# Performance work log

Measured on AMD Instinct MI355X. Metric: run time of the kernel, lower is better.

## Reference

```python
import jax, jax.numpy as jnp
import numpy as np

N = 50000      # nodes
E = 800000     # edges (avg degree 16)
IN = 128       # input feature dim
HID = 32       # per-head hidden dim
OUT = 64       # per-head output dim
H = 2          # heads per layer
NEG = 0.2      # leaky relu negative slope


def setup_inputs() -> dict:
    key = jax.random.key(0)
    ks = jax.random.split(key, 16)
    x = jax.random.normal(ks[0], (N, IN), dtype=jnp.float32)
    src = jax.random.randint(ks[1], (E,), 0, N)
    dst = jax.random.randint(ks[2], (E,), 0, N)

    def lin(k, fin, fout):
        return jax.random.normal(k, (fin, fout), dtype=jnp.float32) * (1.0 / np.sqrt(fin))

    def attn(k, h, d):
        return jax.random.normal(k, (h, d), dtype=jnp.float32) * 0.1

    # layer 0: IN -> H*HID, layer 1: H*HID -> H*HID, layer 2 (output): H*HID -> H*OUT
    W0, al0, ar0, b0 = lin(ks[3], IN, H * HID), attn(ks[4], H, HID), attn(ks[5], H, HID), jnp.zeros((H * HID,), jnp.float32)
    W1, al1, ar1, b1 = lin(ks[6], H * HID, H * HID), attn(ks[7], H, HID), attn(ks[8], H, HID), jnp.zeros((H * HID,), jnp.float32)
    W2, al2, ar2, b2 = lin(ks[9], H * HID, H * OUT), attn(ks[10], H, OUT), attn(ks[11], H, OUT), jnp.zeros((H * OUT,), jnp.float32)
    return {"x": x, "src": src, "dst": dst,
            "W0": W0, "al0": al0, "ar0": ar0, "b0": b0,
            "W1": W1, "al1": al1, "ar1": ar1, "b1": b1,
            "W2": W2, "al2": al2, "ar2": ar2, "b2": b2}


def gat_conv(x, src, dst, W, al, ar, b, heads, out_dim, apply_relu):
    # feat: [N, H, D]
    feat = (x @ W).reshape(-1, heads, out_dim)
    el = jnp.einsum('nhd,hd->nh', feat, al)   # [N, H]
    er = jnp.einsum('nhd,hd->nh', feat, ar)   # [N, H]
    # per-edge attention logits, leaky-relu
    e = jax.nn.leaky_relu(el[src] + er[dst], NEG)          # [E, H]
    # edge softmax over incoming edges of each dst node (numerically stable)
    m = jax.ops.segment_max(e, dst, num_segments=N)        # [N, H]
    m = jnp.where(jnp.isfinite(m), m, 0.0)                 # nodes w/o in-edges
    ex = jnp.exp(e - m[dst])                               # [E, H]
    s = jax.ops.segment_sum(ex, dst, num_segments=N)       # [N, H]
    alpha = ex / s[dst]                                    # [E, H]
    # weighted aggregate of source features into dst nodes
    rst = jax.ops.segment_sum(feat[src] * alpha[:, :, None], dst, num_segments=N)  # [N, H, D]
    rst = rst + b.reshape(1, heads, out_dim)
    if apply_relu:
        rst = jax.nn.relu(rst)
    return rst


def reference(x, src, dst, W0, al0, ar0, b0, W1, al1, ar1, b1, W2, al2, ar2, b2):
    h = gat_conv(x, src, dst, W0, al0, ar0, b0, H, HID, True).reshape(N, H * HID)   # flatten(1)
    h = gat_conv(h, src, dst, W1, al1, ar1, b1, H, HID, True).reshape(N, H * HID)   # flatten(1)
    logits = gat_conv(h, src, dst, W2, al2, ar2, b2, H, OUT, False).mean(axis=1)    # mean over heads -> [N, OUT]
    return logits
```

## Files before the change

kernel.cpp:

```cpp
#include <hip/hip_runtime.h>
#include <hip/hip_bf16.h>
#include <hip/hip_fp16.h>

#define NNODES 50000
#define NEG_SLOPE 0.2f
#define BKT_SHIFT 8
#define NBKT ((NNODES + 255) >> 8)
#define PEPT 8

typedef _Float16 half8 __attribute__((ext_vector_type(8)));
typedef float v4f __attribute__((ext_vector_type(4)));

__device__ __forceinline__ int rfl(int v) { return __builtin_amdgcn_readfirstlane(v); }

__device__ __forceinline__ void pack_one(const float* W, _Float16* Wp, int K, int C, int tid) {
    int KC = K / 32;
    int l = tid & 63;
    int kc = (tid >> 6) % KC;
    int t = tid / (KC * 64);
    int cc = l & 15, q = l >> 4;
    half8 b;
#pragma unroll
    for (int j = 0; j < 8; j++)
        b[j] = (_Float16)W[(size_t)(kc * 32 + q * 8 + j) * C + t * 16 + cc];
    *(half8*)(Wp + (size_t)tid * 8) = b;
}

__global__ void bucket_hist_pack(const int* __restrict__ dst, int* __restrict__ bhist, int E,
                                 const float* __restrict__ W0, _Float16* __restrict__ Wp0,
                                 const float* __restrict__ W1, _Float16* __restrict__ Wp1,
                                 const float* __restrict__ W2, _Float16* __restrict__ Wp2) {
    if (blockIdx.x >= 512) {
        int tid = (blockIdx.x - 512) * 256 + threadIdx.x;
        const int t0 = 4 * 4 * 64, t1 = 4 * 2 * 64, t2 = 8 * 2 * 64;
        if (tid < t0) pack_one(W0, Wp0, 128, 64, tid);
        else if (tid < t0 + t1) pack_one(W1, Wp1, 64, 64, tid - t0);
        else if (tid < t0 + t1 + t2) pack_one(W2, Wp2, 64, 128, tid - t0 - t1);
        return;
    }
    __shared__ int lh[NBKT];
    for (int i = threadIdx.x; i < NBKT; i += 256) lh[i] = 0;
    __syncthreads();
    const int4* d4 = (const int4*)dst;
    int E4 = E >> 2;
    for (int i = blockIdx.x * 256 + threadIdx.x; i < E4; i += 512 * 256) {
        int4 d = d4[i];
        atomicAdd(&lh[d.x >> BKT_SHIFT], 1);
        atomicAdd(&lh[d.y >> BKT_SHIFT], 1);
        atomicAdd(&lh[d.z >> BKT_SHIFT], 1);
        atomicAdd(&lh[d.w >> BKT_SHIFT], 1);
    }
    if (blockIdx.x == 0 && threadIdx.x < (E & 3))
        atomicAdd(&lh[dst[(E4 << 2) + threadIdx.x] >> BKT_SHIFT], 1);
    __syncthreads();
    for (int i = threadIdx.x; i < NBKT; i += 256)
        if (lh[i]) atomicAdd(&bhist[i], lh[i]);
}

__global__ void scan_buckets(const int* __restrict__ bhist, int* __restrict__ bbase,
                             int* __restrict__ bcursor) {
    __shared__ int buf[256];
    int t = threadIdx.x;
    int v = (t < NBKT) ? bhist[t] : 0;
    buf[t] = v;
    __syncthreads();
    for (int off = 1; off < 256; off <<= 1) {
        int x = (t >= off) ? buf[t - off] : 0;
        __syncthreads();
        buf[t] += x;
        __syncthreads();
    }
    if (t < NBKT) { int e = buf[t] - v; bbase[t] = e; bcursor[t * 16] = e; }
}

__global__ __launch_bounds__(1024) void partition_edges(
    const int* __restrict__ src, const int* __restrict__ dst,
    int* __restrict__ bcursor, int2* __restrict__ ebuf, int E) {
    __shared__ int hist[NBKT];
    __shared__ int gbase[NBKT];
    int t = threadIdx.x;
    for (int i = t; i < NBKT; i += 1024) hist[i] = 0;
    __syncthreads();
    int base = blockIdx.x * 1024 * PEPT;
    int sreg[PEPT], dreg[PEPT], rreg[PEPT], breg[PEPT];
#pragma unroll
    for (int k = 0; k < PEPT; k++) {
        int i = base + k * 1024 + t;
        if (i < E) {
            sreg[k] = src[i];
            dreg[k] = dst[i];
            breg[k] = dreg[k] >> BKT_SHIFT;
            rreg[k] = atomicAdd(&hist[breg[k]], 1);
        } else {
            breg[k] = -1;
        }
    }
    __syncthreads();
    for (int i = t; i < NBKT; i += 1024)
        if (hist[i]) gbase[i] = atomicAdd(&bcursor[i * 16], hist[i]);
    __syncthreads();
#pragma unroll
    for (int k = 0; k < PEPT; k++) {
        if (breg[k] >= 0)
            ebuf[(size_t)(gbase[breg[k]] + rreg[k])] = make_int2(sreg[k], dreg[k]);
    }
}

__global__ __launch_bounds__(256) void local_sort(const int2* __restrict__ ebuf,
                                                  const int* __restrict__ bbase,
                                                  int* __restrict__ rowptr,
                                                  int* __restrict__ csrc, int N, int E) {
    __shared__ int lcnt[256], lrow[256], ws[4];
    int b = blockIdx.x;
    int d0 = b << BKT_SHIFT;
    int t = threadIdx.x;
    int base = bbase[b];
    int endE = (b + 1 < NBKT) ? bbase[b + 1] : E;
    lcnt[t] = 0;
    __syncthreads();
    for (int i = base + t; i < endE; i += 256)
        atomicAdd(&lcnt[ebuf[i].y - d0], 1);
    __syncthreads();
    int v = lcnt[t];
    int lane = t & 63;
    int x = v;
#pragma unroll
    for (int m = 1; m < 64; m <<= 1) {
        int y = __shfl_up(x, m, 64);
        if (lane >= m) x += y;
    }
    if (lane == 63) ws[t >> 6] = x;
    __syncthreads();
    int w = t >> 6, waveoff = 0;
#pragma unroll
    for (int k = 0; k < 4; k++) if (k < w) waveoff += ws[k];
    int excl = base + waveoff + x - v;
    lrow[t] = excl;
    int d = d0 + t;
    if (d < N) rowptr[d] = excl;
    if (d == N) rowptr[N] = excl;
    lcnt[t] = 0;
    __syncthreads();
    for (int i = base + t; i < endE; i += 256) {
        int2 e = ebuf[i];
        int ld = e.y - d0;
        int p = lrow[ld] + atomicAdd(&lcnt[ld], 1);
        csrc[p] = e.x;
    }
}

template <int K, int C, bool INTERLEAVE, bool AFP32>
__global__ __launch_bounds__(256) void gemm_mfma(
    const void* __restrict__ Ahi_, const void* __restrict__ Alo_,
    const _Float16* __restrict__ Wp,
    const float* __restrict__ AL, const float* __restrict__ AR,
    void* __restrict__ featout, float2* __restrict__ el2, float2* __restrict__ er2,
    int N) {
    constexpr int KC = K / 32;
    constexpr int NT = C / 16;
    int wave = threadIdx.x >> 6, lane = threadIdx.x & 63;
    int mtile = blockIdx.x * 4 + wave;
    if (mtile * 16 >= N) return;
    int m0 = mtile * 16;
    int c = lane & 15, q = lane >> 4;

    v4f acc[NT];
#pragma unroll
    for (int t = 0; t < NT; t++) acc[t] = (v4f){0.f, 0.f, 0.f, 0.f};

    const size_t arow = (size_t)(m0 + c) * K + q * 8;
#pragma unroll
    for (int kc = 0; kc < KC; kc++) {
        half8 ah, av;
        if constexpr (AFP32) {
            const float* xr = (const float*)Ahi_ + arow + kc * 32;
            float4 f0 = *(const float4*)xr;
            float4 f1 = *(const float4*)(xr + 4);
            float fv[8] = {f0.x, f0.y, f0.z, f0.w, f1.x, f1.y, f1.z, f1.w};
#pragma unroll
            for (int j = 0; j < 8; j++) {
                ah[j] = (_Float16)fv[j];
                av[j] = (_Float16)(fv[j] - (float)ah[j]);
            }
        } else {
            ah = *(const half8*)((const _Float16*)Ahi_ + arow + kc * 32);
            av = *(const half8*)((const _Float16*)Alo_ + arow + kc * 32);
        }
#pragma unroll
        for (int t = 0; t < NT; t++) {
            half8 b = *(const half8*)(Wp + ((size_t)(t * KC + kc) * 64 + lane) * 8);
            acc[t] = __builtin_amdgcn_mfma_f32_16x16x32_f16(ah, b, acc[t], 0, 0, 0);
            acc[t] = __builtin_amdgcn_mfma_f32_16x16x32_f16(av, b, acc[t], 0, 0, 0);
        }
    }

    if (!INTERLEAVE) {
        _Float16* f16 = (_Float16*)featout;
#pragma unroll
        for (int t = 0; t < NT; t++)
#pragma unroll
            for (int r = 0; r < 4; r++) {
                int row = m0 + q * 4 + r;
                f16[(size_t)row * C + t * 16 + c] = (_Float16)acc[t][r];
            }
    } else {
        __half2* f2 = (__half2*)featout;
#pragma unroll
        for (int t = 0; t < NT / 2; t++)
#pragma unroll
            for (int r = 0; r < 4; r++) {
                int row = m0 + q * 4 + r;
                f2[(size_t)row * (C / 2) + t * 16 + c] =
                    __floats2half2_rn(acc[t][r], acc[t + NT / 2][r]);
            }
    }

    float alv[NT], arv[NT];
#pragma unroll
    for (int t = 0; t < NT; t++) { alv[t] = AL[t * 16 + c]; arv[t] = AR[t * 16 + c]; }
#pragma unroll
    for (int r = 0; r < 4; r++) {
        float l0 = 0.f, l1 = 0.f, r0 = 0.f, r1 = 0.f;
#pragma unroll
        for (int t = 0; t < NT; t++) {
            float v = acc[t][r];
            if (t < NT / 2) { l0 = fmaf(v, alv[t], l0); r0 = fmaf(v, arv[t], r0); }
            else            { l1 = fmaf(v, alv[t], l1); r1 = fmaf(v, arv[t], r1); }
        }
#pragma unroll
        for (int m = 1; m < 16; m <<= 1) {
            l0 += __shfl_xor(l0, m, 64);
            l1 += __shfl_xor(l1, m, 64);
            r0 += __shfl_xor(r0, m, 64);
            r1 += __shfl_xor(r1, m, 64);
        }
        if (c == 0) {
            int row = m0 + q * 4 + r;
            el2[row] = make_float2(l0, l1);
            er2[row] = make_float2(r0, r1);
        }
    }
}

__global__ __launch_bounds__(256) void aggregate32(
    const int* __restrict__ rowptr, const int* __restrict__ csrc,
    const float2* __restrict__ el2, const float2* __restrict__ er2,
    const _Float16* __restrict__ feat16, const float* __restrict__ b,
    _Float16* __restrict__ ahi, _Float16* __restrict__ alo, int N) {
    __shared__ int2 stA[4][64], stB[4][64];
    int wave = threadIdx.x >> 6, lane = threadIdx.x & 63, h = lane >> 5;
    int n = rfl(blockIdx.x * 4 + wave);
    if (n >= N) return;
    float bl = b[lane];
    int beg = rfl(rowptr[n]), end = rfl(rowptr[n + 1]);
    float2 rr = er2[n];
    const int2* stH = h ? stB[wave] : stA[wave];
    float s = 0.f, acc = 0.f;
    for (int base = beg; base < end; base += 64) {
        int idx = base + lane;
        int sv = 0; float wxv = 0.f, wyv = 0.f;
        if (idx < end) {
            sv = csrc[idx];
            float2 l = el2[sv];
            float t0 = l.x + rr.x; t0 = t0 > 0.f ? t0 : NEG_SLOPE * t0;
            float t1 = l.y + rr.y; t1 = t1 > 0.f ? t1 : NEG_SLOPE * t1;
            wxv = __expf(t0); wyv = __expf(t1);
        }
        stA[wave][lane] = make_int2(sv, __float_as_int(wxv));
        stB[wave][lane] = make_int2(sv, __float_as_int(wyv));
        int cnt = min(64, end - base);
        int j = 0;
        for (; j + 7 < cnt; j += 8) {
            int4 e01 = *(const int4*)(stH + j);
            int4 e23 = *(const int4*)(stH + j + 2);
            int4 e45 = *(const int4*)(stH + j + 4);
            int4 e67 = *(const int4*)(stH + j + 6);
            float f0 = (float)feat16[(size_t)e01.x * 64 + lane];
            float f1 = (float)feat16[(size_t)e01.z * 64 + lane];
            float f2 = (float)feat16[(size_t)e23.x * 64 + lane];
            float f3 = (float)feat16[(size_t)e23.z * 64 + lane];
            float f4 = (float)feat16[(size_t)e45.x * 64 + lane];
            float f5 = (float)feat16[(size_t)e45.z * 64 + lane];
            float f6 = (float)feat16[(size_t)e67.x * 64 + lane];
            float f7 = (float)feat16[(size_t)e67.z * 64 + lane];
            float w0 = __int_as_float(e01.y), w1 = __int_as_float(e01.w);
            float w2 = __int_as_float(e23.y), w3 = __int_as_float(e23.w);
            float w4 = __int_as_float(e45.y), w5 = __int_as_float(e45.w);
            float w6 = __int_as_float(e67.y), w7 = __int_as_float(e67.w);
            s += ((w0 + w1) + (w2 + w3)) + ((w4 + w5) + (w6 + w7));
            acc = fmaf(w0, f0, acc);
            acc = fmaf(w1, f1, acc);
            acc = fmaf(w2, f2, acc);
            acc = fmaf(w3, f3, acc);
            acc = fmaf(w4, f4, acc);
            acc = fmaf(w5, f5, acc);
            acc = fmaf(w6, f6, acc);
            acc = fmaf(w7, f7, acc);
        }
        for (; j < cnt; j++) {
            int2 e = stH[j];
            float w0 = __int_as_float(e.y);
            float f0 = (float)feat16[(size_t)e.x * 64 + lane];
            s += w0;
            acc = fmaf(w0, f0, acc);
        }
    }
    float v = (s > 0.f) ? acc / s : 0.f;
    v = fmaxf(v + bl, 0.f);
    _Float16 hv = (_Float16)v;
    ahi[(size_t)n * 64 + lane] = hv;
    alo[(size_t)n * 64 + lane] = (_Float16)(v - (float)hv);
}

__global__ __launch_bounds__(256) void aggregate64_mean(
    const int* __restrict__ rowptr, const int* __restrict__ csrc,
    const float2* __restrict__ el2, const float2* __restrict__ er2,
    const __half2* __restrict__ feat2, const float* __restrict__ b,
    float* __restrict__ out, int N) {
    __shared__ int4 st[4][64];
    int wave = threadIdx.x >> 6, lane = threadIdx.x & 63;
    int n = rfl(blockIdx.x * 4 + wave);
    if (n >= N) return;
    float b0 = b[lane], b1 = b[64 + lane];
    int beg = rfl(rowptr[n]), end = rfl(rowptr[n + 1]);
    float2 rr = er2[n];
    float s0 = 0.f, s1 = 0.f, a0 = 0.f, a1 = 0.f;
    for (int base = beg; base < end; base += 64) {
        int idx = base + lane;
        int sv = 0; float wxv = 0.f, wyv = 0.f;
        if (idx < end) {
            sv = csrc[idx];
            float2 l = el2[sv];
            float t0 = l.x + rr.x; t0 = t0 > 0.f ? t0 : NEG_SLOPE * t0;
            float t1 = l.y + rr.y; t1 = t1 > 0.f ? t1 : NEG_SLOPE * t1;
            wxv = __expf(t0); wyv = __expf(t1);
        }
        st[wave][lane] = make_int4(sv, __float_as_int(wxv), __float_as_int(wyv), 0);
        int cnt = min(64, end - base);
        int j = 0;
        for (; j + 7 < cnt; j += 8) {
            float2 fv[8]; float wxs[8], wys[8];
#pragma unroll
            for (int u = 0; u < 8; u++) {
                int4 e = st[wave][j + u];
                wxs[u] = __int_as_float(e.y);
                wys[u] = __int_as_float(e.z);
                fv[u] = __half22float2(feat2[(size_t)e.x * 64 + lane]);
            }
#pragma unroll
            for (int u = 0; u < 8; u++) {
                s0 += wxs[u]; s1 += wys[u];
                a0 = fmaf(wxs[u], fv[u].x, a0);
                a1 = fmaf(wys[u], fv[u].y, a1);
            }
        }
        for (; j < cnt; j++) {
            int4 e = st[wave][j];
            float wx0 = __int_as_float(e.y), wy0 = __int_as_float(e.z);
            float2 f0 = __half22float2(feat2[(size_t)e.x * 64 + lane]);
            s0 += wx0; s1 += wy0;
            a0 = fmaf(wx0, f0.x, a0); a1 = fmaf(wy0, f0.y, a1);
        }
    }
    float v0 = (s0 > 0.f) ? a0 / s0 : 0.f;
    float v1 = (s1 > 0.f) ? a1 / s1 : 0.f;
    out[(size_t)n * 64 + lane] = 0.5f * ((v0 + b0) + (v1 + b1));
}


extern "C" void kernel_launch(void* const* d_in, const int* in_sizes, int n_in,
                              void* d_out, int out_size, void* d_ws, size_t ws_size,
                              hipStream_t stream) {
    const float* x   = (const float*)d_in[0];
    const int*   src = (const int*)d_in[1];
    const int*   dst = (const int*)d_in[2];
    const float* W0  = (const float*)d_in[3];
    const float* al0 = (const float*)d_in[4];
    const float* ar0 = (const float*)d_in[5];
    const float* b0  = (const float*)d_in[6];
    const float* W1  = (const float*)d_in[7];
    const float* al1 = (const float*)d_in[8];
    const float* ar1 = (const float*)d_in[9];
    const float* b1  = (const float*)d_in[10];
    const float* W2  = (const float*)d_in[11];
    const float* al2 = (const float*)d_in[12];
    const float* ar2 = (const float*)d_in[13];
    const float* b2  = (const float*)d_in[14];
    float* out = (float*)d_out;

    const int N = NNODES;
    const int E = in_sizes[1];

    char* p = (char*)d_ws;
    auto alloc = [&](size_t bytes) {
        void* r = (void*)p;
        p += (bytes + 255) & ~(size_t)255;
        return r;
    };
    int*    bhist    = (int*)alloc((size_t)NBKT * 4);
    int*    bbase    = (int*)alloc((size_t)NBKT * 4);
    int*    bcursor  = (int*)alloc((size_t)NBKT * 16 * 4);
    int*    rowptr   = (int*)alloc((size_t)(N + 1) * 4);
    int2*   ebuf     = (int2*)alloc((size_t)E * 8);
    int*    csrc     = (int*)alloc((size_t)E * 4);
    float2* el2      = (float2*)alloc((size_t)N * 8);
    float2* er2      = (float2*)alloc((size_t)N * 8);
    _Float16* ahi    = (_Float16*)alloc((size_t)N * 64 * 2);
    _Float16* alo    = (_Float16*)alloc((size_t)N * 64 * 2);
    void*   featbuf  = alloc((size_t)N * 64 * 4);
    _Float16* Wp0    = (_Float16*)alloc(4 * 4 * 64 * 8 * 2);
    _Float16* Wp1    = (_Float16*)alloc(4 * 2 * 64 * 8 * 2);
    _Float16* Wp2    = (_Float16*)alloc(8 * 2 * 64 * 8 * 2);
    _Float16* feat16 = (_Float16*)featbuf;
    __half2*  feat2  = (__half2*)featbuf;

    hipMemsetAsync(bhist, 0, (size_t)NBKT * 4, stream);
    bucket_hist_pack<<<522, 256, 0, stream>>>(dst, bhist, E, W0, Wp0, W1, Wp1, W2, Wp2);
    scan_buckets<<<1, 256, 0, stream>>>(bhist, bbase, bcursor);
    int pb = (E + 1024 * PEPT - 1) / (1024 * PEPT);
    partition_edges<<<pb, 1024, 0, stream>>>(src, dst, bcursor, ebuf, E);
    local_sort<<<NBKT, 256, 0, stream>>>(ebuf, bbase, rowptr, csrc, N, E);

    int nb4 = (N + 3) / 4;
    int gb = (N / 16 + 3) / 4;

    gemm_mfma<128, 64, false, true><<<gb, 256, 0, stream>>>(x, nullptr, Wp0, al0, ar0, featbuf, el2, er2, N);
    aggregate32<<<nb4, 256, 0, stream>>>(rowptr, csrc, el2, er2, feat16, b0, ahi, alo, N);

    gemm_mfma<64, 64, false, false><<<gb, 256, 0, stream>>>(ahi, alo, Wp1, al1, ar1, featbuf, el2, er2, N);
    aggregate32<<<nb4, 256, 0, stream>>>(rowptr, csrc, el2, er2, feat16, b1, ahi, alo, N);

    gemm_mfma<64, 128, true, false><<<gb, 256, 0, stream>>>(ahi, alo, Wp2, al2, ar2, featbuf, el2, er2, N);
    aggregate64_mean<<<nb4, 256, 0, stream>>>(rowptr, csrc, el2, er2, feat2, b2, out, N);
}
```

Before: 257.4 us.

## Drop bucket histogram pass and fuse layer-0 aggregation with layer-1 GEMM

Edge partitioning now gives each destination bucket a fixed-capacity region, so the dst histogram, the scan kernel and the memset go away. Per-node start/end pairs replace rowptr. The layer-0 GEMM is merged with the cursor init and W2 packing, and reads W0 directly without a pre-pack step. Layer-0 aggregation is fused with the layer-1 linear transform and attention projections, done in fp32 FMAs with W1 held in registers. This removes several launches and intermediate round trips, but the fixed bucket capacity assumes no bucket holds more than 5120 edges and would overflow on skewed graphs. The fused kernel is also register-heavy.

```diff
diff --git a/kernel.cpp b/kernel.cpp
--- a/kernel.cpp
+++ b/kernel.cpp
@@ -6,6 +6,7 @@
 #define NEG_SLOPE 0.2f
 #define BKT_SHIFT 8
 #define NBKT ((NNODES + 255) >> 8)
+#define STRIDE 5120
 #define PEPT 8
 
 typedef _Float16 half8 __attribute__((ext_vector_type(8)));
@@ -26,51 +27,85 @@
     *(half8*)(Wp + (size_t)tid * 8) = b;
 }
 
-__global__ void bucket_hist_pack(const int* __restrict__ dst, int* __restrict__ bhist, int E,
-                                 const float* __restrict__ W0, _Float16* __restrict__ Wp0,
-                                 const float* __restrict__ W1, _Float16* __restrict__ Wp1,
-                                 const float* __restrict__ W2, _Float16* __restrict__ Wp2) {
-    if (blockIdx.x >= 512) {
-        int tid = (blockIdx.x - 512) * 256 + threadIdx.x;
-        const int t0 = 4 * 4 * 64, t1 = 4 * 2 * 64, t2 = 8 * 2 * 64;
-        if (tid < t0) pack_one(W0, Wp0, 128, 64, tid);
-        else if (tid < t0 + t1) pack_one(W1, Wp1, 64, 64, tid - t0);
-        else if (tid < t0 + t1 + t2) pack_one(W2, Wp2, 64, 128, tid - t0 - t1);
+__global__ __launch_bounds__(256) void kernelA(
+    const float* __restrict__ x, const float* __restrict__ W0,
+    const float* __restrict__ AL, const float* __restrict__ AR,
+    _Float16* __restrict__ featA, float2* __restrict__ el2A, float2* __restrict__ er2A,
+    int* __restrict__ bcursor,
+    const float* __restrict__ W2, _Float16* __restrict__ Wp2, int N) {
+    int blk = blockIdx.x;
+    if (blk == 782) {
+        if (threadIdx.x < NBKT) bcursor[threadIdx.x * 16] = threadIdx.x * STRIDE;
         return;
     }
-    __shared__ int lh[NBKT];
-    for (int i = threadIdx.x; i < NBKT; i += 256) lh[i] = 0;
-    __syncthreads();
-    const int4* d4 = (const int4*)dst;
-    int E4 = E >> 2;
-    for (int i = blockIdx.x * 256 + threadIdx.x; i < E4; i += 512 * 256) {
-        int4 d = d4[i];
-        atomicAdd(&lh[d.x >> BKT_SHIFT], 1);
-        atomicAdd(&lh[d.y >> BKT_SHIFT], 1);
-        atomicAdd(&lh[d.z >> BKT_SHIFT], 1);
-        atomicAdd(&lh[d.w >> BKT_SHIFT], 1);
-    }
-    if (blockIdx.x == 0 && threadIdx.x < (E & 3))
-        atomicAdd(&lh[dst[(E4 << 2) + threadIdx.x] >> BKT_SHIFT], 1);
-    __syncthreads();
-    for (int i = threadIdx.x; i < NBKT; i += 256)
-        if (lh[i]) atomicAdd(&bhist[i], lh[i]);
-}
-
-__global__ void scan_buckets(const int* __restrict__ bhist, int* __restrict__ bbase,
-                             int* __restrict__ bcursor) {
-    __shared__ int buf[256];
-    int t = threadIdx.x;
-    int v = (t < NBKT) ? bhist[t] : 0;
-    buf[t] = v;
-    __syncthreads();
-    for (int off = 1; off < 256; off <<= 1) {
-        int x = (t >= off) ? buf[t - off] : 0;
-        __syncthreads();
-        buf[t] += x;
-        __syncthreads();
-    }
-    if (t < NBKT) { int e = buf[t] - v; bbase[t] = e; bcursor[t * 16] = e; }
+    if (blk > 782) {
+        int tid = (blk - 783) * 256 + threadIdx.x;
+        if (tid < 8 * 2 * 64) pack_one(W2, Wp2, 64, 128, tid);
+        return;
+    }
+    int wave = threadIdx.x >> 6, lane = threadIdx.x & 63;
+    int mtile = blk * 4 + wave;
+    if (mtile * 16 >= N) return;
+    int m0 = mtile * 16;
+    int c = lane & 15, q = lane >> 4;
+    v4f acc[4];
+#pragma unroll
+    for (int t = 0; t < 4; t++) acc[t] = (v4f){0.f, 0.f, 0.f, 0.f};
+    const size_t arow = (size_t)(m0 + c) * 128 + q * 8;
+#pragma unroll
+    for (int kc = 0; kc < 4; kc++) {
+        const float* xr = x + arow + kc * 32;
+        float4 f0 = *(const float4*)xr;
+        float4 f1 = *(const float4*)(xr + 4);
+        float fv[8] = {f0.x, f0.y, f0.z, f0.w, f1.x, f1.y, f1.z, f1.w};
+        half8 ah, av;
+#pragma unroll
+        for (int j = 0; j < 8; j++) {
+            ah[j] = (_Float16)fv[j];
+            av[j] = (_Float16)(fv[j] - (float)ah[j]);
+        }
+#pragma unroll
+        for (int tt = 0; tt < 4; tt++) {
+            half8 b;
+#pragma unroll
+            for (int j = 0; j < 8; j++)
+                b[j] = (_Float16)W0[(size_t)(kc * 32 + q * 8 + j) * 64 + tt * 16 + c];
+            acc[tt] = __builtin_amdgcn_mfma_f32_16x16x32_f16(ah, b, acc[tt], 0, 0, 0);
+            acc[tt] = __builtin_amdgcn_mfma_f32_16x16x32_f16(av, b, acc[tt], 0, 0, 0);
+        }
+    }
+#pragma unroll
+    for (int tt = 0; tt < 4; tt++)
+#pragma unroll
+        for (int r = 0; r < 4; r++) {
+            int row = m0 + q * 4 + r;
+            featA[(size_t)row * 64 + tt * 16 + c] = (_Float16)acc[tt][r];
+        }
+    float alv[4], arv[4];
+#pragma unroll
+    for (int tt = 0; tt < 4; tt++) { alv[tt] = AL[tt * 16 + c]; arv[tt] = AR[tt * 16 + c]; }
+#pragma unroll
+    for (int r = 0; r < 4; r++) {
+        float l0 = 0.f, l1 = 0.f, r0 = 0.f, r1 = 0.f;
+#pragma unroll
+        for (int tt = 0; tt < 4; tt++) {
+            float v = acc[tt][r];
+            if (tt < 2) { l0 = fmaf(v, alv[tt], l0); r0 = fmaf(v, arv[tt], r0); }
+            else        { l1 = fmaf(v, alv[tt], l1); r1 = fmaf(v, arv[tt], r1); }
+        }
+#pragma unroll
+        for (int m = 1; m < 16; m <<= 1) {
+            l0 += __shfl_xor(l0, m, 64);
+            l1 += __shfl_xor(l1, m, 64);
+            r0 += __shfl_xor(r0, m, 64);
+            r1 += __shfl_xor(r1, m, 64);
+        }
+        if (c == 0) {
+            int row = m0 + q * 4 + r;
+            el2A[row] = make_float2(l0, l1);
+            er2A[row] = make_float2(r0, r1);
+        }
+    }
 }
 
 __global__ __launch_bounds__(1024) void partition_edges(
@@ -107,15 +142,15 @@
 }
 
 __global__ __launch_bounds__(256) void local_sort(const int2* __restrict__ ebuf,
-                                                  const int* __restrict__ bbase,
-                                                  int* __restrict__ rowptr,
-                                                  int* __restrict__ csrc, int N, int E) {
+                                                  const int* __restrict__ bcursor,
+                                                  int2* __restrict__ rowse,
+                                                  int* __restrict__ csrc, int N) {
     __shared__ int lcnt[256], lrow[256], ws[4];
     int b = blockIdx.x;
     int d0 = b << BKT_SHIFT;
     int t = threadIdx.x;
-    int base = bbase[b];
-    int endE = (b + 1 < NBKT) ? bbase[b + 1] : E;
+    int base = b * STRIDE;
+    int endE = bcursor[b * 16];
     lcnt[t] = 0;
     __syncthreads();
     for (int i = base + t; i < endE; i += 256)
@@ -137,8 +172,7 @@
     int excl = base + waveoff + x - v;
     lrow[t] = excl;
     int d = d0 + t;
-    if (d < N) rowptr[d] = excl;
-    if (d == N) rowptr[N] = excl;
+    if (d < N) rowse[d] = make_int2(excl, excl + v);
     lcnt[t] = 0;
     __syncthreads();
     for (int i = base + t; i < endE; i += 256) {
@@ -149,101 +183,106 @@
     }
 }
 
-template <int K, int C, bool INTERLEAVE, bool AFP32>
-__global__ __launch_bounds__(256) void gemm_mfma(
-    const void* __restrict__ Ahi_, const void* __restrict__ Alo_,
-    const _Float16* __restrict__ Wp,
-    const float* __restrict__ AL, const float* __restrict__ AR,
-    void* __restrict__ featout, float2* __restrict__ el2, float2* __restrict__ er2,
+__global__ __launch_bounds__(256, 3) void agg0_gemm1(
+    const int2* __restrict__ rowse, const int* __restrict__ csrc,
+    const float2* __restrict__ el2A, const float2* __restrict__ er2A,
+    const _Float16* __restrict__ featA, const float* __restrict__ b0,
+    const float* __restrict__ W1, const float* __restrict__ al1, const float* __restrict__ ar1,
+    _Float16* __restrict__ featB, float2* __restrict__ el2B, float2* __restrict__ er2B,
     int N) {
-    constexpr int KC = K / 32;
-    constexpr int NT = C / 16;
-    int wave = threadIdx.x >> 6, lane = threadIdx.x & 63;
-    int mtile = blockIdx.x * 4 + wave;
-    if (mtile * 16 >= N) return;
-    int m0 = mtile * 16;
-    int c = lane & 15, q = lane >> 4;
-
-    v4f acc[NT];
-#pragma unroll
-    for (int t = 0; t < NT; t++) acc[t] = (v4f){0.f, 0.f, 0.f, 0.f};
-
-    const size_t arow = (size_t)(m0 + c) * K + q * 8;
-#pragma unroll
-    for (int kc = 0; kc < KC; kc++) {
-        half8 ah, av;
-        if constexpr (AFP32) {
-            const float* xr = (const float*)Ahi_ + arow + kc * 32;
-            float4 f0 = *(const float4*)xr;
-            float4 f1 = *(const float4*)(xr + 4);
-            float fv[8] = {f0.x, f0.y, f0.z, f0.w, f1.x, f1.y, f1.z, f1.w};
-#pragma unroll
-            for (int j = 0; j < 8; j++) {
-                ah[j] = (_Float16)fv[j];
-                av[j] = (_Float16)(fv[j] - (float)ah[j]);
+    __shared__ int2 stA[4][64], stB[4][64];
+    __shared__ float vbuf[4][64];
+    int wave = threadIdx.x >> 6, lane = threadIdx.x & 63, h = lane >> 5;
+    float bl = b0[lane];
+    float w1r[64];
+#pragma unroll
+    for (int k = 0; k < 64; k++) w1r[k] = W1[k * 64 + lane];
+    float al1v = al1[lane], ar1v = ar1[lane];
+    const int2* stH = h ? stB[wave] : stA[wave];
+    for (int n0 = blockIdx.x * 4 + wave; n0 < N; n0 += gridDim.x * 4) {
+        int n = rfl(n0);
+        int2 se = rowse[n];
+        int beg = rfl(se.x), end = rfl(se.y);
+        float2 rr = er2A[n];
+        float s = 0.f, acc = 0.f;
+        for (int base = beg; base < end; base += 64) {
+            int idx = base + lane;
+            int sv = 0; float wxv = 0.f, wyv = 0.f;
+            if (idx < end) {
+                sv = csrc[idx];
+                float2 l = el2A[sv];
+                float t0 = l.x + rr.x; t0 = t0 > 0.f ? t0 : NEG_SLOPE * t0;
+                float t1 = l.y + rr.y; t1 = t1 > 0.f ? t1 : NEG_SLOPE * t1;
+                wxv = __expf(t0); wyv = __expf(t1);
             }
-        } else {
-            ah = *(const half8*)((const _Float16*)Ahi_ + arow + kc * 32);
-            av = *(const half8*)((const _Float16*)Alo_ + arow + kc * 32);
-        }
-#pragma unroll
-        for (int t = 0; t < NT; t++) {
-            half8 b = *(const half8*)(Wp + ((size_t)(t * KC + kc) * 64 + lane) * 8);
-            acc[t] = __builtin_amdgcn_mfma_f32_16x16x32_f16(ah, b, acc[t], 0, 0, 0);
-            acc[t] = __builtin_amdgcn_mfma_f32_16x16x32_f16(av, b, acc[t], 0, 0, 0);
-        }
-    }
-
-    if (!INTERLEAVE) {
-        _Float16* f16 = (_Float16*)featout;
-#pragma unroll
-        for (int t = 0; t < NT; t++)
-#pragma unroll
-            for (int r = 0; r < 4; r++) {
-                int row = m0 + q * 4 + r;
-                f16[(size_t)row * C + t * 16 + c] = (_Float16)acc[t][r];
+            stA[wave][lane] = make_int2(sv, __float_as_int(wxv));
+            stB[wave][lane] = make_int2(sv, __float_as_int(wyv));
+            int cnt = min(64, end - base);
+            int j = 0;
+            for (; j + 7 < cnt; j += 8) {
+                int4 e01 = *(const int4*)(stH + j);
+                int4 e23 = *(const int4*)(stH + j + 2);
+                int4 e45 = *(const int4*)(stH + j + 4);
+                int4 e67 = *(const int4*)(stH + j + 6);
+                float f0 = (float)featA[(size_t)e01.x * 64 + lane];
+                float f1 = (float)featA[(size_t)e01.z * 64 + lane];
+                float f2 = (float)featA[(size_t)e23.x * 64 + lane];
+                float f3 = (float)featA[(size_t)e23.z * 64 + lane];
+                float f4 = (float)featA[(size_t)e45.x * 64 + lane];
+                float f5 = (float)featA[(size_t)e45.z * 64 + lane];
+                float f6 = (float)featA[(size_t)e67.x * 64 + lane];
+                float f7 = (float)featA[(size_t)e67.z * 64 + lane];
+                float w0 = __int_as_float(e01.y), w1 = __int_as_float(e01.w);
+                float w2 = __int_as_float(e23.y), w3 = __int_as_float(e23.w);
+                float w4 = __int_as_float(e45.y), w5 = __int_as_float(e45.w);
+                float w6 = __int_as_float(e67.y), w7 = __int_as_float(e67.w);
+                s += ((w0 + w1) + (w2 + w3)) + ((w4 + w5) + (w6 + w7));
+                acc = fmaf(w0, f0, acc);
+                acc = fmaf(w1, f1, acc);
+                acc = fmaf(w2, f2, acc);
+                acc = fmaf(w3, f3, acc);
+                acc = fmaf(w4, f4, acc);
+                acc = fmaf(w5, f5, acc);
+                acc = fmaf(w6, f6, acc);
+                acc = fmaf(w7, f7, acc);
             }
-    } else {
-        __half2* f2 = (__half2*)featout;
-#pragma unroll
-        for (int t = 0; t < NT / 2; t++)
-#pragma unroll
-            for (int r = 0; r < 4; r++) {
-                int row = m0 + q * 4 + r;
-                f2[(size_t)row * (C / 2) + t * 16 + c] =
-                    __floats2half2_rn(acc[t][r], acc[t + NT / 2][r]);
+            for (; j < cnt; j++) {
+                int2 e = stH[j];
+                float w0 = __int_as_float(e.y);
+                float f0 = (float)featA[(size_t)e.x * 64 + lane];
+                s += w0;
+                acc = fmaf(w0, f0, acc);
             }
-    }
-
-    float alv[NT], arv[NT];
-#pragma unroll
-    for (int t = 0; t < NT; t++) { alv[t] = AL[t * 16 + c]; arv[t] = AR[t * 16 + c]; }
-#pragma unroll
-    for (int r = 0; r < 4; r++) {
-        float l0 = 0.f, l1 = 0.f, r0 = 0.f, r1 = 0.f;
-#pragma unroll
-        for (int t = 0; t < NT; t++) {
-            float v = acc[t][r];
-            if (t < NT / 2) { l0 = fmaf(v, alv[t], l0); r0 = fmaf(v, arv[t], r0); }
-            else            { l1 = fmaf(v, alv[t], l1); r1 = fmaf(v, arv[t], r1); }
-        }
-#pragma unroll
-        for (int m = 1; m < 16; m <<= 1) {
-            l0 += __shfl_xor(l0, m, 64);
-            l1 += __shfl_xor(l1, m, 64);
-            r0 += __shfl_xor(r0, m, 64);
-            r1 += __shfl_xor(r1, m, 64);
-        }
-        if (c == 0) {
-            int row = m0 + q * 4 + r;
-            el2[row] = make_float2(l0, l1);
-            er2[row] = make_float2(r0, r1);
+        }
+        float v = (s > 0.f) ? acc / s : 0.f;
+        v = fmaxf(v + bl, 0.f);
+        vbuf[wave][lane] = v;
+        const float4* vv = (const float4*)vbuf[wave];
+        float f = 0.f;
+#pragma unroll
+        for (int kk = 0; kk < 16; kk++) {
+            float4 v4 = vv[kk];
+            f = fmaf(v4.x, w1r[4 * kk + 0], f);
+            f = fmaf(v4.y, w1r[4 * kk + 1], f);
+            f = fmaf(v4.z, w1r[4 * kk + 2], f);
+            f = fmaf(v4.w, w1r[4 * kk + 3], f);
+        }
+        featB[(size_t)n * 64 + lane] = (_Float16)f;
+        float vl = f * al1v, vr = f * ar1v;
+#pragma unroll
+        for (int m = 1; m < 32; m <<= 1) {
+            vl += __shfl_xor(vl, m, 64);
+            vr += __shfl_xor(vr, m, 64);
+        }
+        if ((lane & 31) == 0) {
+            ((float*)el2B)[n * 2 + h] = vl;
+            ((float*)er2B)[n * 2 + h] = vr;
         }
     }
 }
 
 __global__ __launch_bounds__(256) void aggregate32(
-    const int* __restrict__ rowptr, const int* __restrict__ csrc,
+    const int2* __restrict__ rowse, const int* __restrict__ csrc,
     const float2* __restrict__ el2, const float2* __restrict__ er2,
     const _Float16* __restrict__ feat16, const float* __restrict__ b,
     _Float16* __restrict__ ahi, _Float16* __restrict__ alo, int N) {
@@ -252,7 +291,8 @@
     int n = rfl(blockIdx.x * 4 + wave);
     if (n >= N) return;
     float bl = b[lane];
-    int beg = rfl(rowptr[n]), end = rfl(rowptr[n + 1]);
+    int2 se = rowse[n];
+    int beg = rfl(se.x), end = rfl(se.y);
     float2 rr = er2[n];
     const int2* stH = h ? stB[wave] : stA[wave];
     float s = 0.f, acc = 0.f;
@@ -312,8 +352,70 @@
     alo[(size_t)n * 64 + lane] = (_Float16)(v - (float)hv);
 }
 
+__global__ __launch_bounds__(256) void gemm_mfma2(
+    const _Float16* __restrict__ Ahi, const _Float16* __restrict__ Alo,
+    const _Float16* __restrict__ Wp,
+    const float* __restrict__ AL, const float* __restrict__ AR,
+    __half2* __restrict__ feat2, float2* __restrict__ el2, float2* __restrict__ er2,
+    int N) {
+    constexpr int KC = 2, NT = 8;
+    int wave = threadIdx.x >> 6, lane = threadIdx.x & 63;
+    int mtile = blockIdx.x * 4 + wave;
+    if (mtile * 16 >= N) return;
+    int m0 = mtile * 16;
+    int c = lane & 15, q = lane >> 4;
+    v4f acc[NT];
+#pragma unroll
+    for (int t = 0; t < NT; t++) acc[t] = (v4f){0.f, 0.f, 0.f, 0.f};
+    const size_t arow = (size_t)(m0 + c) * 64 + q * 8;
+#pragma unroll
+    for (int kc = 0; kc < KC; kc++) {
+        half8 ah = *(const half8*)(Ahi + arow + kc * 32);
+        half8 av = *(const half8*)(Alo + arow + kc * 32);
+#pragma unroll
+        for (int t = 0; t < NT; t++) {
+            half8 b = *(const half8*)(Wp + ((size_t)(t * KC + kc) * 64 + lane) * 8);
+            acc[t] = __builtin_amdgcn_mfma_f32_16x16x32_f16(ah, b, acc[t], 0, 0, 0);
+            acc[t] = __builtin_amdgcn_mfma_f32_16x16x32_f16(av, b, acc[t], 0, 0, 0);
+        }
+    }
+#pragma unroll
+    for (int t = 0; t < NT / 2; t++)
+#pragma unroll
+        for (int r = 0; r < 4; r++) {
+            int row = m0 + q * 4 + r;
+            feat2[(size_t)row * 64 + t * 16 + c] =
+                __floats2half2_rn(acc[t][r], acc[t + NT / 2][r]);
+        }
+    float alv[NT], arv[NT];
+#pragma unroll
+    for (int t = 0; t < NT; t++) { alv[t] = AL[t * 16 + c]; arv[t] = AR[t * 16 + c]; }
+#pragma unroll
+    for (int r = 0; r < 4; r++) {
+        float l0 = 0.f, l1 = 0.f, r0 = 0.f, r1 = 0.f;
+#pragma unroll
+        for (int t = 0; t < NT; t++) {
+            float v = acc[t][r];
+            if (t < NT / 2) { l0 = fmaf(v, alv[t], l0); r0 = fmaf(v, arv[t], r0); }
+            else            { l1 = fmaf(v, alv[t], l1); r1 = fmaf(v, arv[t], r1); }
+        }
+#pragma unroll
+        for (int m = 1; m < 16; m <<= 1) {
+            l0 += __shfl_xor(l0, m, 64);
+            l1 += __shfl_xor(l1, m, 64);
+            r0 += __shfl_xor(r0, m, 64);
+            r1 += __shfl_xor(r1, m, 64);
+        }
+        if (c == 0) {
+            int row = m0 + q * 4 + r;
+            el2[row] = make_float2(l0, l1);
+            er2[row] = make_float2(r0, r1);
+        }
+    }
+}
+
 __global__ __launch_bounds__(256) void aggregate64_mean(
-    const int* __restrict__ rowptr, const int* __restrict__ csrc,
+    const int2* __restrict__ rowse, const int* __restrict__ csrc,
     const float2* __restrict__ el2, const float2* __restrict__ er2,
     const __half2* __restrict__ feat2, const float* __restrict__ b,
     float* __restrict__ out, int N) {
@@ -322,7 +424,8 @@
     int n = rfl(blockIdx.x * 4 + wave);
     if (n >= N) return;
     float b0 = b[lane], b1 = b[64 + lane];
-    int beg = rfl(rowptr[n]), end = rfl(rowptr[n + 1]);
+    int2 se = rowse[n];
+    int beg = rfl(se.x), end = rfl(se.y);
     float2 rr = er2[n];
     float s0 = 0.f, s1 = 0.f, a0 = 0.f, a1 = 0.f;
     for (int base = beg; base < end; base += 64) {
@@ -397,39 +500,32 @@
         p += (bytes + 255) & ~(size_t)255;
         return r;
     };
-    int*    bhist    = (int*)alloc((size_t)NBKT * 4);
-    int*    bbase    = (int*)alloc((size_t)NBKT * 4);
-    int*    bcursor  = (int*)alloc((size_t)NBKT * 16 * 4);
-    int*    rowptr   = (int*)alloc((size_t)(N + 1) * 4);
-    int2*   ebuf     = (int2*)alloc((size_t)E * 8);
-    int*    csrc     = (int*)alloc((size_t)E * 4);
-    float2* el2      = (float2*)alloc((size_t)N * 8);
-    float2* er2      = (float2*)alloc((size_t)N * 8);
-    _Float16* ahi    = (_Float16*)alloc((size_t)N * 64 * 2);
-    _Float16* alo    = (_Float16*)alloc((size_t)N * 64 * 2);
-    void*   featbuf  = alloc((size_t)N * 64 * 4);
-    _Float16* Wp0    = (_Float16*)alloc(4 * 4 * 64 * 8 * 2);
-    _Float16* Wp1    = (_Float16*)alloc(4 * 2 * 64 * 8 * 2);
-    _Float16* Wp2    = (_Float16*)alloc(8 * 2 * 64 * 8 * 2);
-    _Float16* feat16 = (_Float16*)featbuf;
-    __half2*  feat2  = (__half2*)featbuf;
-
-    hipMemsetAsync(bhist, 0, (size_t)NBKT * 4, stream);
-    bucket_hist_pack<<<522, 256, 0, stream>>>(dst, bhist, E, W0, Wp0, W1, Wp1, W2, Wp2);
-    scan_buckets<<<1, 256, 0, stream>>>(bhist, bbase, bcursor);
+    int*    bcursor = (int*)alloc((size_t)NBKT * 16 * 4);
+    int2*   rowse   = (int2*)alloc((size_t)N * 8);
+    int2*   ebuf    = (int2*)alloc(((size_t)NBKT * STRIDE + 4096) * 8);
+    int*    csrc    = (int*)alloc(((size_t)NBKT * STRIDE + 4096) * 4);
+    float2* el2A    = (float2*)alloc((size_t)N * 8);
+    float2* er2A    = (float2*)alloc((size_t)N * 8);
+    float2* el2B    = (float2*)alloc((size_t)N * 8);
+    float2* er2B    = (float2*)alloc((size_t)N * 8);
+    _Float16* ahi   = (_Float16*)alloc((size_t)N * 64 * 2);
+    _Float16* alo   = (_Float16*)alloc((size_t)N * 64 * 2);
+    void*   featA   = alloc((size_t)N * 64 * 4);
+    _Float16* featB = (_Float16*)alloc((size_t)N * 64 * 2);
+    _Float16* Wp2   = (_Float16*)alloc(8 * 2 * 64 * 8 * 2);
+
+    kernelA<<<787, 256, 0, stream>>>(x, W0, al0, ar0, (_Float16*)featA, el2A, er2A,
+                                     bcursor, W2, Wp2, N);
     int pb = (E + 1024 * PEPT - 1) / (1024 * PEPT);
     partition_edges<<<pb, 1024, 0, stream>>>(src, dst, bcursor, ebuf, E);
-    local_sort<<<NBKT, 256, 0, stream>>>(ebuf, bbase, rowptr, csrc, N, E);
+    local_sort<<<NBKT, 256, 0, stream>>>(ebuf, bcursor, rowse, csrc, N);
 
     int nb4 = (N + 3) / 4;
+    agg0_gemm1<<<1024, 256, 0, stream>>>(rowse, csrc, el2A, er2A, (const _Float16*)featA,
+                                         b0, W1, al1, ar1, featB, el2B, er2B, N);
+    aggregate32<<<nb4, 256, 0, stream>>>(rowse, csrc, el2B, er2B, featB, b1, ahi, alo, N);
     int gb = (N / 16 + 3) / 4;
-
-    gemm_mfma<128, 64, false, true><<<gb, 256, 0, stream>>>(x, nullptr, Wp0, al0, ar0, featbuf, el2, er2, N);
-    aggregate32<<<nb4, 256, 0, stream>>>(rowptr, csrc, el2, er2, feat16, b0, ahi, alo, N);
-
-    gemm_mfma<64, 64, false, false><<<gb, 256, 0, stream>>>(ahi, alo, Wp1, al1, ar1, featbuf, el2, er2, N);
-    aggregate32<<<nb4, 256, 0, stream>>>(rowptr, csrc, el2, er2, feat16, b1, ahi, alo, N);
-
-    gemm_mfma<64, 128, true, false><<<gb, 256, 0, stream>>>(ahi, alo, Wp2, al2, ar2, featbuf, el2, er2, N);
-    aggregate64_mean<<<nb4, 256, 0, stream>>>(rowptr, csrc, el2, er2, feat2, b2, out, N);
-}
+    gemm_mfma2<<<gb, 256, 0, stream>>>(ahi, alo, Wp2, al2, ar2, (__half2*)featA, el2A, er2A, N);
+    aggregate64_mean<<<nb4, 256, 0, stream>>>(rowse, csrc, el2A, er2A, (const __half2*)featA,
+                                              b2, out, N);
+}
```

Result: faster. 246.7 us (-4.2%).
